# Optimization experiments

Hardware: AMD Instinct MI355X
Metric: run time of the kernel (lower is better)

## Reference

```python
import math
import jax, jax.numpy as jnp
import numpy as np

B, C, H, W = 2, 256, 256, 256
TH, TW = 256, 256
U = V = 2            # window_size
PE_DIM = 256
DIM = 256
HEADS = 8
TEMP = 10000.0


def sine_pe(y, x, num_pos_feats, temp, card):
    """Faithful port of get_sine_position_encoding (use_norm=True)."""
    eps = 1e-6
    scale = 2.0 * math.pi
    y = y / (card[0] + eps) * scale
    x = x / (card[1] + eps) * scale
    dt = jnp.arange(num_pos_feats, dtype=jnp.float32)
    dim_t = temp ** (2.0 * jnp.floor(dt / 2.0) / num_pos_feats)
    px = x[..., None] / dim_t
    py = y[..., None] / dim_t

    def interleave(p):
        s = jnp.stack((jnp.sin(p[..., 0::2]), jnp.cos(p[..., 1::2])), axis=-1)
        return s.reshape(s.shape[:-2] + (-1,))

    return jnp.concatenate((interleave(py), interleave(px)), axis=-1)


def setup_inputs() -> dict:
    key = jax.random.key(0)
    ks = jax.random.split(key, 8)
    return {
        "feat_supp": jax.random.normal(ks[0], (B, C, H, W), jnp.float32),
        "offset": jax.random.normal(ks[1], (B, TH, TW, 2), jnp.float32) * 2.0,
        "Wq": jax.random.normal(ks[2], (DIM, PE_DIM), jnp.float32) * 0.02,
        "bq": jax.random.normal(ks[3], (DIM,), jnp.float32) * 0.02,
        "Wk": jax.random.normal(ks[4], (DIM, PE_DIM), jnp.float32) * 0.02,
        "bk": jax.random.normal(ks[5], (DIM,), jnp.float32) * 0.02,
        "Wv": jax.random.normal(ks[6], (DIM, PE_DIM), jnp.float32) * 0.02,
        "bv": jax.random.normal(ks[7], (DIM,), jnp.float32) * 0.02,
    }


def reference(feat_supp, offset, Wq, bq, Wk, bk, Wv, bv):
    UV = U * V
    THW = TH * TW
    Dh = DIM // HEADS
    attn_scale = Dh ** (-0.5)
    d = PE_DIM // C  # = 1 here

    # --- warp grid: integer window corners + fractional residual ---
    tgt = jnp.stack(jnp.meshgrid(jnp.arange(TH), jnp.arange(TW), indexing='ij'), axis=-1)  # [TH,TW,2]
    win = jnp.stack(jnp.meshgrid(jnp.arange(U), jnp.arange(V), indexing='ij'), axis=-1)    # [U,V,2]
    full = tgt[None].astype(jnp.float32) + offset[..., ::-1]            # [B,TH,TW,2]
    intg = jnp.floor(full).astype(jnp.int32)
    deci = (full - intg.astype(full.dtype)).reshape(B, THW, 2)          # fractional part
    idx = (intg[:, :, :, None, None, :] + win[None, None, None]).reshape(B, THW * UV, 2)

    # --- duplicate-padding gather (gather_hw) ---
    h_idx = jnp.clip(idx[..., 0], 0, H - 1)
    w_idx = jnp.clip(idx[..., 1], 0, W - 1)
    feat = feat_supp.transpose(0, 2, 3, 1).reshape(B, H * W, C)
    lin = h_idx * W + w_idx                                             # [B, THW*UV]
    feat_warp = jnp.take_along_axis(feat, lin[:, :, None], axis=1)      # [B, THW*UV, C]
    feat_warp_ori = feat_warp.reshape(B, THW, UV, C, 1)

    # --- sine PE on window coords (card = window_size - 1) ---
    ye, xe = jnp.meshgrid(jnp.arange(U, dtype=jnp.float32), jnp.arange(V, dtype=jnp.float32), indexing='ij')
    pos_bias = sine_pe(ye.reshape(1, -1), xe.reshape(1, -1), PE_DIM // 2, TEMP, (U - 1, V - 1))  # [1,UV,PE_DIM]
    pe_warp = pos_bias.reshape(1, 1, UV, C, d)
    fw = (feat_warp_ori + pe_warp).reshape(B, THW, UV, PE_DIM)

    # --- query features: window mean + sine PE of fractional offset (card = window_size) ---
    feat_base = feat_warp_ori[..., 0].mean(axis=2)                      # [B,THW,C]
    pe_curr = sine_pe(deci[..., 0], deci[..., 1], PE_DIM // 2, TEMP, (U, V)).reshape(B, THW, C, d)
    fb = (feat_base[..., None] + pe_curr).reshape(B, THW, PE_DIM)

    # --- cross attention: 1 query vs UV keys per target pixel ---
    q = (fb @ Wq.T + bq).reshape(B, THW, HEADS, Dh)
    k = (fw @ Wk.T + bk).reshape(B, THW, UV, HEADS, Dh)
    v = (fw @ Wv.T + bv).reshape(B, THW, UV, HEADS, Dh)
    attn = jnp.einsum('bthd,btuhd->bthu', q * attn_scale, k)
    attn = jax.nn.softmax(attn, axis=-1)
    out = jnp.einsum('bthu,btuhd->bthd', attn, v).reshape(B, TH, TW, DIM)
    return out.transpose(0, 3, 1, 2)                                    # [B, DIM, TH, TW]
```

## Files before the change

kernel.cpp:

```cpp
#include <hip/hip_runtime.h>


using short8 = __attribute__((ext_vector_type(8))) short;
using uint4v = __attribute__((ext_vector_type(4))) unsigned;
using f32x4  = __attribute__((ext_vector_type(4))) float;
typedef unsigned short u16;

#define LOG2_1E4 13.287712379549449f
#define TWO_PI   6.283185307179586f
#define ATT_SCL  0.17677669529663687f

__device__ __forceinline__ float bs2f(u16 s) {
    unsigned u = ((unsigned)s) << 16;
    float f; __builtin_memcpy(&f, &u, 4); return f;
}
__device__ __forceinline__ u16 f2bs(float f) {
    unsigned u; __builtin_memcpy(&u, &f, 4);
    u += 0x7fffu + ((u >> 16) & 1u);
    return (u16)(u >> 16);
}
__device__ __forceinline__ unsigned cvt_pk_bf16(float lo, float hi) {
    unsigned r;
    asm("v_cvt_pk_bf16_f32 %0, %1, %2" : "=v"(r) : "v"(lo), "v"(hi));
    return r;
}

__device__ __forceinline__ int probe_is_f32(const u16* offs_raw) {
    const int lane = threadIdx.x & 63;
    const float v = bs2f(offs_raw[lane * 2]);
    const float av = fabsf(v);
    const bool insane = !(av >= 1e-3f && av <= 1000.0f);
    return __popcll(__ballot(insane)) >= 16 ? 1 : 0;
}

__global__ __launch_bounds__(256) void irm_canon(
    const void* offs_raw, const void* Wq_r, const void* bq_r,
    const void* Wk_r, const void* bk_r, const void* Wv_r, const void* bv_r,
    unsigned char* canon)
{
    const int is_f32 = probe_is_f32((const u16*)offs_raw);
    float* offsC = (float*)canon;
    u16* WqC = (u16*)(canon + (1u << 20));
    u16* WkC = (u16*)(canon + (1u << 20) + (1u << 17));
    u16* WvC = (u16*)(canon + (1u << 20) + (2u << 17));
    u16* bqC = (u16*)(canon + (1u << 20) + (3u << 17));
    u16* bkC = bqC + 256;
    u16* bvC = bkC + 256;

    const int gid = blockIdx.x * 256 + threadIdx.x;
    if (gid < 262144) {
        offsC[gid] = is_f32 ? ((const float*)offs_raw)[gid]
                            : bs2f(((const u16*)offs_raw)[gid]);
    } else if (gid < 262144 + 3 * 65536) {
        const int r = gid - 262144, w = r >> 16, i = r & 65535;
        const void* src = (w == 0) ? Wq_r : (w == 1) ? Wk_r : Wv_r;
        u16*       dst  = (w == 0) ? WqC  : (w == 1) ? WkC  : WvC;
        dst[i] = is_f32 ? f2bs(((const float*)src)[i]) : ((const u16*)src)[i];
    } else if (gid < 262144 + 3 * 65536 + 3 * 256) {
        const int r = gid - 262144 - 3 * 65536, w = r >> 8, i = r & 255;
        const void* src = (w == 0) ? bq_r : (w == 1) ? bk_r : bv_r;
        u16*       dst  = (w == 0) ? bqC  : (w == 1) ? bkC  : bvC;
        dst[i] = is_f32 ? f2bs(((const float*)src)[i]) : ((const u16*)src)[i];
    }
}

__global__ __launch_bounds__(256) void irm_transpose(const void* __restrict__ feat_raw,
                                                     const u16* __restrict__ offs_raw,
                                                     u16* __restrict__ featT) {
    const int is_f32 = probe_is_f32(offs_raw);
    __shared__ u16 tile[64][72];
    const int b   = blockIdx.z;
    const int c0  = blockIdx.y << 6;
    const int hw0 = blockIdx.x << 6;
    const int tid = threadIdx.x;
    const int r    = tid >> 4;
    const int col4 = (tid & 15) << 2;
    #pragma unroll
    for (int it = 0; it < 4; ++it) {
        const int c = (it << 4) + r;
        const size_t idx = ((size_t)((b << 8) + c0 + c) << 16) + hw0 + col4;
        ushort4 o;
        if (is_f32) {
            const float4 v = *(const float4*)((const float*)feat_raw + idx);
            const unsigned lo = cvt_pk_bf16(v.x, v.y);
            const unsigned hi = cvt_pk_bf16(v.z, v.w);
            o.x = (u16)(lo & 0xffffu); o.y = (u16)(lo >> 16);
            o.z = (u16)(hi & 0xffffu); o.w = (u16)(hi >> 16);
        } else {
            o = *(const ushort4*)((const u16*)feat_raw + idx);
        }
        *(ushort4*)&tile[c][col4 ^ (((c >> 3) & 7) << 3)] = o;
    }
    __syncthreads();
    const int s = tid & 7;
    const int m = tid >> 3;
    #pragma unroll
    for (int it2 = 0; it2 < 2; ++it2) {
        const int hw = (it2 << 5) + m;
        short8 o;
        #pragma unroll
        for (int k = 0; k < 8; ++k) {
            const int c = (s << 3) + k;
            o[k] = (short)tile[c][hw ^ (((c >> 3) & 7) << 3)];
        }
        u16* dst = featT + (((size_t)((b << 16) + hw0 + hw)) << 8) + c0 + (s << 3);
        *(short8*)dst = o;
    }
}

__global__ __launch_bounds__(256, 3) void irm_main(
    const void* __restrict__ fsrc,
    const int transposed,
    const u16* __restrict__ offs_raw,
    const float* __restrict__ offsC,
    const u16* __restrict__ Wq, const u16* __restrict__ bq,
    const u16* __restrict__ Wk, const u16* __restrict__ bk_unused,
    const u16* __restrict__ Wv, const u16* __restrict__ bv,
    void* __restrict__ out_raw)
{
    const int is_f32 = probe_is_f32(offs_raw);

    __shared__ __align__(16) unsigned char smem[52992];
    float* pe1    = (float*)smem;
    float* invtab = (float*)(smem + 1024);
    float* sA     = (float*)smem;
    u16*   sFw    = (u16*)(smem + 2304);
    u16*   sV     = (u16*)(smem + 2304);
    u16*   sFb    = (u16*)(smem + 36096);
    u16*   sQ     = (u16*)(smem + 44544);

    const int tid = threadIdx.x;
    const int raw = blockIdx.x;
    const int wq_ = ((raw & 7) << 10) | (raw >> 3);
    const int b   = wq_ >> 12;
    const int t0  = (wq_ & 4095) << 4;

    const int p0 = tid >> 4;
    const int cx = tid & 15;
    const int t  = t0 + p0;
    const float offx = offsC[((((size_t)b << 16) + (size_t)t) << 1) + 0];
    const float offy = offsC[((((size_t)b << 16) + (size_t)t) << 1) + 1];

    {
        const int c = tid;
        const int j = (c & 127) >> 1;
        const float invt = exp2f(-(float)j * (LOG2_1E4 / 64.0f));
        const float arg = (TWO_PI / (1.0f + 1e-6f)) * invt;
        pe1[c]    = (c & 1) ? __cosf(arg) : __sinf(arg);
        invtab[c] = invt;
    }
    __syncthreads();

    {
        const int ty = t >> 8, tx = t & 255;
        const float fy = (float)ty + offy;
        const float fx = (float)tx + offx;
        const float fiy = floorf(fy), fix = floorf(fx);
        const int iy = (int)fiy, ix = (int)fix;
        const float dy = fy - fiy, dx = fx - fix;

        int lin4[4];
        #pragma unroll
        for (int u = 0; u < 4; ++u) {
            int hy = iy + (u >> 1); hy = hy < 0 ? 0 : (hy > 255 ? 255 : hy);
            int wx = ix + (u & 1);  wx = wx < 0 ? 0 : (wx > 255 ? 255 : wx);
            lin4[u] = (hy << 8) | wx;
        }

        short8 g[4][2];
        if (transposed) {
            #pragma unroll
            for (int u = 0; u < 4; ++u) {
                const u16* src = (const u16*)fsrc +
                    ((((size_t)(b << 16)) + (size_t)lin4[u]) << 8) + (cx << 4);
                g[u][0] = *(const short8*)(src);
                g[u][1] = *(const short8*)(src + 8);
            }
        } else {
            #pragma unroll
            for (int u = 0; u < 4; ++u) {
                #pragma unroll
                for (int i = 0; i < 8; ++i) {
                    const size_t i0 = (((size_t)((b << 8) + (cx << 4) + i)) << 16) + lin4[u];
                    const size_t i1 = (((size_t)((b << 8) + (cx << 4) + 8 + i)) << 16) + lin4[u];
                    g[u][0][i] = is_f32 ? (short)f2bs(((const float*)fsrc)[i0]) : (short)((const u16*)fsrc)[i0];
                    g[u][1][i] = is_f32 ? (short)f2bs(((const float*)fsrc)[i1]) : (short)((const u16*)fsrc)[i1];
                }
            }
        }

        float pe1v[16], invtv[16];
        #pragma unroll
        for (int i = 0; i < 16; ++i) {
            pe1v[i]  = pe1[(cx << 4) + i];
            invtv[i] = invtab[(cx << 4) + i];
        }

        const bool hi_half = (cx >= 8);
        float gsum[16];
        #pragma unroll
        for (int i = 0; i < 16; ++i) gsum[i] = 0.0f;

        #pragma unroll
        for (int u = 0; u < 4; ++u) {
            const bool sel = hi_half ? (bool)(u & 1) : (bool)(u >> 1);
            unsigned pk[8];
            #pragma unroll
            for (int i2 = 0; i2 < 8; ++i2) {
                float w2[2];
                #pragma unroll
                for (int k = 0; k < 2; ++k) {
                    const int i = i2 * 2 + k;
                    const float f = bs2f((u16)g[u][i >> 3][i & 7]);
                    gsum[i] += f;
                    const float pz = (i & 1) ? 1.0f : 0.0f;
                    w2[k] = f + (sel ? pe1v[i] : pz);
                }
                pk[i2] = cvt_pk_bf16(w2[0], w2[1]);
            }
            const uint4v lo = {pk[0], pk[1], pk[2], pk[3]};
            const uint4v hi = {pk[4], pk[5], pk[6], pk[7]};
            *(uint4v*)&sFw[((p0 << 2) + u) * 264 + (cx << 4)]     = lo;
            *(uint4v*)&sFw[((p0 << 2) + u) * 264 + (cx << 4) + 8] = hi;
        }

        const float ys = dy * (TWO_PI / (2.0f + 1e-6f));
        const float xs = dx * (TWO_PI / (2.0f + 1e-6f));
        const float sxy = hi_half ? xs : ys;
        unsigned qk[8];
        #pragma unroll
        for (int i2 = 0; i2 < 8; ++i2) {
            float v2[2];
            #pragma unroll
            for (int k = 0; k < 2; ++k) {
                const int i = i2 * 2 + k;
                const float arg = sxy * invtv[i];
                const float pe = (i & 1) ? __cosf(arg) : __sinf(arg);
                v2[k] = gsum[i] * 0.25f + pe;
            }
            qk[i2] = cvt_pk_bf16(v2[0], v2[1]);
        }
        const uint4v qlo = {qk[0], qk[1], qk[2], qk[3]};
        const uint4v qhi = {qk[4], qk[5], qk[6], qk[7]};
        *(uint4v*)&sFb[p0 * 264 + (cx << 4)]     = qlo;
        *(uint4v*)&sFb[p0 * 264 + (cx << 4) + 8] = qhi;
    }
    __syncthreads();

    const int lane = tid & 63;
    const int wv   = tid >> 6;
    const int c15  = lane & 15;
    const int qd   = lane >> 4;
    const int colbase = wv << 6;
    const f32x4 zero4 = {0.f, 0.f, 0.f, 0.f};

    {
        f32x4 accQ[4];
        #pragma unroll
        for (int nt = 0; nt < 4; ++nt) accQ[nt] = zero4;
        #pragma unroll
        for (int ks = 0; ks < 8; ++ks) {
            short8 aq = *(const short8*)&sFb[c15 * 264 + ks * 32 + qd * 8];
            #pragma unroll
            for (int nt = 0; nt < 4; ++nt) {
                short8 bw = *(const short8*)&Wq[(colbase + nt * 16 + c15) * 256 + ks * 32 + qd * 8];
                accQ[nt] = __builtin_amdgcn_mfma_f32_16x16x32_bf16(aq, bw, accQ[nt], 0, 0, 0);
            }
        }
        #pragma unroll
        for (int nt = 0; nt < 4; ++nt) {
            const int n = colbase + nt * 16 + c15;
            const float bias = bs2f(bq[n]);
            #pragma unroll
            for (int rp = 0; rp < 2; ++rp) {
                const unsigned pk = cvt_pk_bf16(accQ[nt][2 * rp] + bias, accQ[nt][2 * rp + 1] + bias);
                sQ[(qd * 4 + 2 * rp)     * 264 + n] = (u16)(pk & 0xffffu);
                sQ[(qd * 4 + 2 * rp + 1) * 264 + n] = (u16)(pk >> 16);
            }
        }
    }
    asm volatile("" ::: "memory");

    f32x4 accK[4][4];
    #pragma unroll
    for (int m = 0; m < 4; ++m)
        #pragma unroll
        for (int nt = 0; nt < 4; ++nt) accK[m][nt] = zero4;
    #pragma unroll
    for (int ks = 0; ks < 8; ++ks) {
        short8 af[4], bfr[4];
        #pragma unroll
        for (int m = 0; m < 4; ++m)
            af[m] = *(const short8*)&sFw[(m * 16 + c15) * 264 + ks * 32 + qd * 8];
        #pragma unroll
        for (int nt = 0; nt < 4; ++nt)
            bfr[nt] = *(const short8*)&Wk[(colbase + nt * 16 + c15) * 256 + ks * 32 + qd * 8];
        #pragma unroll
        for (int m = 0; m < 4; ++m)
            #pragma unroll
            for (int nt = 0; nt < 4; ++nt)
                accK[m][nt] = __builtin_amdgcn_mfma_f32_16x16x32_bf16(af[m], bfr[nt], accK[m][nt], 0, 0, 0);
    }

    {
        float part[4][4][2];
        #pragma unroll
        for (int m = 0; m < 4; ++m)
            #pragma unroll
            for (int r = 0; r < 4; ++r) { part[m][r][0] = 0.f; part[m][r][1] = 0.f; }
        #pragma unroll
        for (int m = 0; m < 4; ++m) {
            #pragma unroll
            for (int nt = 0; nt < 4; ++nt) {
                const float qv = bs2f(sQ[(4 * m + qd) * 264 + colbase + nt * 16 + c15]);
                #pragma unroll
                for (int r = 0; r < 4; ++r)
                    part[m][r][nt >> 1] += accK[m][nt][r] * qv;
            }
        }
        #pragma unroll
        for (int m = 0; m < 4; ++m)
            #pragma unroll
            for (int r = 0; r < 4; ++r)
                #pragma unroll
                for (int h2 = 0; h2 < 2; ++h2) {
                    float v = part[m][r][h2];
                    v += __shfl_xor(v, 1);
                    v += __shfl_xor(v, 2);
                    v += __shfl_xor(v, 4);
                    v += __shfl_xor(v, 8);
                    part[m][r][h2] = v;
                }
        auto smax_write = [&](const float (&pm)[4][2], const int p) {
            #pragma unroll
            for (int h2 = 0; h2 < 2; ++h2) {
                const float l0 = pm[0][h2] * ATT_SCL, l1 = pm[1][h2] * ATT_SCL;
                const float l2 = pm[2][h2] * ATT_SCL, l3 = pm[3][h2] * ATT_SCL;
                const float mx = fmaxf(fmaxf(l0, l1), fmaxf(l2, l3));
                const float e0 = __expf(l0 - mx), e1 = __expf(l1 - mx);
                const float e2 = __expf(l2 - mx), e3 = __expf(l3 - mx);
                const float inv = __fdividef(1.0f, e0 + e1 + e2 + e3);
                float* ap = &sA[p * 36 + ((wv << 1) + h2) * 4];
                ap[0] = e0 * inv; ap[1] = e1 * inv; ap[2] = e2 * inv; ap[3] = e3 * inv;
            }
        };
        if      (c15 == 0) { smax_write(part[0], qd);     smax_write(part[1], 4 + qd);  }
        else if (c15 == 8) { smax_write(part[2], 8 + qd); smax_write(part[3], 12 + qd); }
    }

    f32x4 accV[4][4];
    #pragma unroll
    for (int m = 0; m < 4; ++m)
        #pragma unroll
        for (int nt = 0; nt < 4; ++nt) accV[m][nt] = zero4;
    #pragma unroll
    for (int ks = 0; ks < 8; ++ks) {
        short8 af[4], bfr[4];
        #pragma unroll
        for (int m = 0; m < 4; ++m)
            af[m] = *(const short8*)&sFw[(m * 16 + c15) * 264 + ks * 32 + qd * 8];
        #pragma unroll
        for (int nt = 0; nt < 4; ++nt)
            bfr[nt] = *(const short8*)&Wv[(colbase + nt * 16 + c15) * 256 + ks * 32 + qd * 8];
        #pragma unroll
        for (int m = 0; m < 4; ++m)
            #pragma unroll
            for (int nt = 0; nt < 4; ++nt)
                accV[m][nt] = __builtin_amdgcn_mfma_f32_16x16x32_bf16(af[m], bfr[nt], accV[m][nt], 0, 0, 0);
    }
    __syncthreads();

    #pragma unroll
    for (int nt = 0; nt < 4; ++nt) {
        const int n = colbase + nt * 16 + c15;
        const float bias = bs2f(bv[n]);
        #pragma unroll
        for (int m = 0; m < 4; ++m) {
            #pragma unroll
            for (int rp = 0; rp < 2; ++rp) {
                const int row = m * 16 + qd * 4 + 2 * rp;
                const int ns = n ^ (((row >> 2) & 7) << 3);
                const unsigned pk = cvt_pk_bf16(accV[m][nt][2 * rp] + bias, accV[m][nt][2 * rp + 1] + bias);
                sV[row * 264 + ns]       = (u16)(pk & 0xffffu);
                sV[(row + 1) * 264 + ns] = (u16)(pk >> 16);
            }
        }
    }
    __syncthreads();

    {
        const int p  = tid & 15;
        const int h  = (tid >> 4) & 7;
        const int dh = tid >> 7;
        const f32x4 a4 = *(const f32x4*)&sA[p * 36 + h * 4];
        float acc[16];
        #pragma unroll
        for (int i = 0; i < 16; ++i) acc[i] = 0.0f;
        #pragma unroll
        for (int u = 0; u < 4; ++u) {
            const int row = p * 4 + u;
            const int f = ((row >> 2) & 7) << 3;
            const int cb = h * 32 + dh * 16;
            const short8 v0 = *(const short8*)&sV[row * 264 + (cb ^ f)];
            const short8 v1 = *(const short8*)&sV[row * 264 + ((cb + 8) ^ f)];
            const float a = a4[u];
            #pragma unroll
            for (int i = 0; i < 8; ++i) {
                acc[i]     += a * bs2f((u16)v0[i]);
                acc[i + 8] += a * bs2f((u16)v1[i]);
            }
        }
        const size_t base = (((size_t)((b << 8) + h * 32 + dh * 16)) << 16) + t0 + p;
        if (is_f32) {
            float* dst = (float*)out_raw + base;
            #pragma unroll
            for (int i = 0; i < 16; ++i)
                __builtin_nontemporal_store(acc[i], dst + ((size_t)i << 16));
        } else {
            u16* dst = (u16*)out_raw + base;
            #pragma unroll
            for (int i = 0; i < 16; ++i)
                __builtin_nontemporal_store(f2bs(acc[i]), dst + ((size_t)i << 16));
        }
    }
}

extern "C" void kernel_launch(void* const* d_in, const int* in_sizes, int n_in,
                              void* d_out, int out_size, void* d_ws, size_t ws_size,
                              hipStream_t stream) {
    const size_t FEATT_BYTES = (size_t)1 << 26;
    const size_t CANON_BYTES = (1u << 20) + (3u << 17) + 3 * 512;
    const int use_t = (ws_size >= FEATT_BYTES + CANON_BYTES) ? 1 : 0;

    unsigned char* ws    = (unsigned char*)d_ws;
    unsigned char* canon = ws + (use_t ? FEATT_BYTES : 0);
    float* offsC = (float*)canon;
    u16* WqC = (u16*)(canon + (1u << 20));
    u16* WkC = (u16*)(canon + (1u << 20) + (1u << 17));
    u16* WvC = (u16*)(canon + (1u << 20) + (2u << 17));
    u16* bqC = (u16*)(canon + (1u << 20) + (3u << 17));
    u16* bkC = bqC + 256;
    u16* bvC = bkC + 256;

    irm_canon<<<1795, 256, 0, stream>>>(d_in[1], d_in[2], d_in[3], d_in[4],
                                        d_in[5], d_in[6], d_in[7], canon);
    if (use_t)
        irm_transpose<<<dim3(1024, 4, 2), 256, 0, stream>>>(d_in[0], (const u16*)d_in[1], (u16*)ws);
    irm_main<<<dim3(8192), 256, 0, stream>>>(use_t ? (const void*)ws : d_in[0], use_t,
                                             (const u16*)d_in[1], offsC,
                                             WqC, bqC, WkC, bkC, WvC, bvC, d_out);
}
```

Measured before the change: 610.6 us.

## Transpose MFMA operands to keep Q/K/V in registers and drop LDS round-trips

Swaps the MFMA operand roles so weights are the A operand and features the B operand. Each lane then holds Q, K and V for one pixel column, which lets attention logits, softmax and the weighted V sum run entirely in registers with small cross-lane shuffles. The sQ/sA/sV shared buffers, the extra barriers and the per-block PE table setup (now computed per thread with sincos) go away, and the feature tiles use an XOR-swizzled layout. Shared memory drops enough to raise the occupancy hint to 4 blocks per CU. In exchange, output stores become strided per lane and are no longer nontemporal, and register pressure may limit the higher occupancy.

```diff
diff --git a/kernel.cpp b/kernel.cpp
--- a/kernel.cpp
+++ b/kernel.cpp
@@ -108,7 +108,7 @@
     }
 }
 
-__global__ __launch_bounds__(256, 3) void irm_main(
+__global__ __launch_bounds__(256, 4) void irm_main(
     const void* __restrict__ fsrc,
     const int transposed,
     const u16* __restrict__ offs_raw,
@@ -120,14 +120,9 @@
 {
     const int is_f32 = probe_is_f32(offs_raw);
 
-    __shared__ __align__(16) unsigned char smem[52992];
-    float* pe1    = (float*)smem;
-    float* invtab = (float*)(smem + 1024);
-    float* sA     = (float*)smem;
-    u16*   sFw    = (u16*)(smem + 2304);
-    u16*   sV     = (u16*)(smem + 2304);
-    u16*   sFb    = (u16*)(smem + 36096);
-    u16*   sQ     = (u16*)(smem + 44544);
+    __shared__ __align__(16) unsigned char smem[40960];
+    u16* sFb = (u16*)smem;
+    u16* sFw = (u16*)(smem + 8192);
 
     const int tid = threadIdx.x;
     const int raw = blockIdx.x;
@@ -140,16 +135,6 @@
     const int t  = t0 + p0;
     const float offx = offsC[((((size_t)b << 16) + (size_t)t) << 1) + 0];
     const float offy = offsC[((((size_t)b << 16) + (size_t)t) << 1) + 1];
-
-    {
-        const int c = tid;
-        const int j = (c & 127) >> 1;
-        const float invt = exp2f(-(float)j * (LOG2_1E4 / 64.0f));
-        const float arg = (TWO_PI / (1.0f + 1e-6f)) * invt;
-        pe1[c]    = (c & 1) ? __cosf(arg) : __sinf(arg);
-        invtab[c] = invt;
-    }
-    __syncthreads();
 
     {
         const int ty = t >> 8, tx = t & 255;
@@ -189,11 +174,13 @@
             }
         }
 
-        float pe1v[16], invtv[16];
-        #pragma unroll
-        for (int i = 0; i < 16; ++i) {
-            pe1v[i]  = pe1[(cx << 4) + i];
-            invtv[i] = invtab[(cx << 4) + i];
+        float invt[8], s1[8], c1[8];
+        #pragma unroll
+        for (int a = 0; a < 8; ++a) {
+            const int j = ((cx << 3) + a) & 63;
+            invt[a] = exp2f(-(float)j * (LOG2_1E4 / 64.0f));
+            const float arg = (TWO_PI / (1.0f + 1e-6f)) * invt[a];
+            __sincosf(arg, &s1[a], &c1[a]);
         }
 
         const bool hi_half = (cx >= 8);
@@ -206,22 +193,21 @@
             const bool sel = hi_half ? (bool)(u & 1) : (bool)(u >> 1);
             unsigned pk[8];
             #pragma unroll
-            for (int i2 = 0; i2 < 8; ++i2) {
-                float w2[2];
-                #pragma unroll
-                for (int k = 0; k < 2; ++k) {
-                    const int i = i2 * 2 + k;
-                    const float f = bs2f((u16)g[u][i >> 3][i & 7]);
-                    gsum[i] += f;
-                    const float pz = (i & 1) ? 1.0f : 0.0f;
-                    w2[k] = f + (sel ? pe1v[i] : pz);
-                }
-                pk[i2] = cvt_pk_bf16(w2[0], w2[1]);
-            }
+            for (int a = 0; a < 8; ++a) {
+                const float f0 = bs2f((u16)g[u][a >> 2][(2 * a) & 7]);
+                const float f1 = bs2f((u16)g[u][a >> 2][(2 * a + 1) & 7]);
+                gsum[2 * a]     += f0;
+                gsum[2 * a + 1] += f1;
+                const float w0 = f0 + (sel ? s1[a] : 0.0f);
+                const float w1 = f1 + (sel ? c1[a] : 1.0f);
+                pk[a] = cvt_pk_bf16(w0, w1);
+            }
+            const int row = (p0 << 2) + u;
+            const int rp  = row ^ ((row >> 3) & 7);
             const uint4v lo = {pk[0], pk[1], pk[2], pk[3]};
             const uint4v hi = {pk[4], pk[5], pk[6], pk[7]};
-            *(uint4v*)&sFw[((p0 << 2) + u) * 264 + (cx << 4)]     = lo;
-            *(uint4v*)&sFw[((p0 << 2) + u) * 264 + (cx << 4) + 8] = hi;
+            *(uint4v*)&sFw[(((2 * cx) * 64 + rp)) * 8]     = lo;
+            *(uint4v*)&sFw[(((2 * cx + 1) * 64 + rp)) * 8] = hi;
         }
 
         const float ys = dy * (TWO_PI / (2.0f + 1e-6f));
@@ -229,21 +215,16 @@
         const float sxy = hi_half ? xs : ys;
         unsigned qk[8];
         #pragma unroll
-        for (int i2 = 0; i2 < 8; ++i2) {
-            float v2[2];
-            #pragma unroll
-            for (int k = 0; k < 2; ++k) {
-                const int i = i2 * 2 + k;
-                const float arg = sxy * invtv[i];
-                const float pe = (i & 1) ? __cosf(arg) : __sinf(arg);
-                v2[k] = gsum[i] * 0.25f + pe;
-            }
-            qk[i2] = cvt_pk_bf16(v2[0], v2[1]);
-        }
+        for (int a = 0; a < 8; ++a) {
+            float s2, c2;
+            __sincosf(sxy * invt[a], &s2, &c2);
+            qk[a] = cvt_pk_bf16(gsum[2 * a] * 0.25f + s2, gsum[2 * a + 1] * 0.25f + c2);
+        }
+        const int rb = p0 ^ (cx & 7);
         const uint4v qlo = {qk[0], qk[1], qk[2], qk[3]};
         const uint4v qhi = {qk[4], qk[5], qk[6], qk[7]};
-        *(uint4v*)&sFb[p0 * 264 + (cx << 4)]     = qlo;
-        *(uint4v*)&sFb[p0 * 264 + (cx << 4) + 8] = qhi;
+        *(uint4v*)&sFb[((2 * cx) * 16 + rb) * 8]     = qlo;
+        *(uint4v*)&sFb[((2 * cx + 1) * 16 + rb) * 8] = qhi;
     }
     __syncthreads();
 
@@ -253,174 +234,119 @@
     const int qd   = lane >> 4;
     const int colbase = wv << 6;
     const f32x4 zero4 = {0.f, 0.f, 0.f, 0.f};
-
+    const int kwkey = (c15 >> 1) & 7;
+    const int krow0 = 4 * c15;
+
+    f32x4 accQt[4];
+    #pragma unroll
+    for (int nt = 0; nt < 4; ++nt) accQt[nt] = zero4;
+    #pragma unroll
+    for (int ks = 0; ks < 8; ++ks) {
+        const int gidx = ks * 4 + qd;
+        const short8 bfb = *(const short8*)&sFb[(gidx * 16 + (c15 ^ ((gidx >> 1) & 7))) * 8];
+        #pragma unroll
+        for (int nt = 0; nt < 4; ++nt) {
+            const short8 aw = *(const short8*)&Wq[(colbase + nt * 16 + c15) * 256 + ks * 32 + qd * 8];
+            accQt[nt] = __builtin_amdgcn_mfma_f32_16x16x32_bf16(aw, bfb, accQt[nt], 0, 0, 0);
+        }
+    }
+    #pragma unroll
+    for (int nt = 0; nt < 4; ++nt) {
+        const ushort4 b4 = *(const ushort4*)&bq[colbase + nt * 16 + qd * 4];
+        accQt[nt][0] += bs2f(b4.x); accQt[nt][1] += bs2f(b4.y);
+        accQt[nt][2] += bs2f(b4.z); accQt[nt][3] += bs2f(b4.w);
+    }
+
+    f32x4 accKt[4][4];
+    #pragma unroll
+    for (int u = 0; u < 4; ++u)
+        #pragma unroll
+        for (int nt = 0; nt < 4; ++nt) accKt[u][nt] = zero4;
+    #pragma unroll
+    for (int ks = 0; ks < 8; ++ks) {
+        short8 aw[4];
+        #pragma unroll
+        for (int nt = 0; nt < 4; ++nt)
+            aw[nt] = *(const short8*)&Wk[(colbase + nt * 16 + c15) * 256 + ks * 32 + qd * 8];
+        #pragma unroll
+        for (int u = 0; u < 4; ++u) {
+            const short8 bf = *(const short8*)&sFw[((ks * 4 + qd) * 64 + ((krow0 + u) ^ kwkey)) * 8];
+            #pragma unroll
+            for (int nt = 0; nt < 4; ++nt)
+                accKt[u][nt] = __builtin_amdgcn_mfma_f32_16x16x32_bf16(aw[nt], bf, accKt[u][nt], 0, 0, 0);
+        }
+    }
+
+    float att[4][2];
     {
-        f32x4 accQ[4];
-        #pragma unroll
-        for (int nt = 0; nt < 4; ++nt) accQ[nt] = zero4;
-        #pragma unroll
-        for (int ks = 0; ks < 8; ++ks) {
-            short8 aq = *(const short8*)&sFb[c15 * 264 + ks * 32 + qd * 8];
-            #pragma unroll
-            for (int nt = 0; nt < 4; ++nt) {
-                short8 bw = *(const short8*)&Wq[(colbase + nt * 16 + c15) * 256 + ks * 32 + qd * 8];
-                accQ[nt] = __builtin_amdgcn_mfma_f32_16x16x32_bf16(aq, bw, accQ[nt], 0, 0, 0);
-            }
-        }
-        #pragma unroll
-        for (int nt = 0; nt < 4; ++nt) {
-            const int n = colbase + nt * 16 + c15;
-            const float bias = bs2f(bq[n]);
-            #pragma unroll
-            for (int rp = 0; rp < 2; ++rp) {
-                const unsigned pk = cvt_pk_bf16(accQ[nt][2 * rp] + bias, accQ[nt][2 * rp + 1] + bias);
-                sQ[(qd * 4 + 2 * rp)     * 264 + n] = (u16)(pk & 0xffffu);
-                sQ[(qd * 4 + 2 * rp + 1) * 264 + n] = (u16)(pk >> 16);
-            }
-        }
-    }
-    asm volatile("" ::: "memory");
-
-    f32x4 accK[4][4];
-    #pragma unroll
-    for (int m = 0; m < 4; ++m)
-        #pragma unroll
-        for (int nt = 0; nt < 4; ++nt) accK[m][nt] = zero4;
+        float lg[4][2];
+        #pragma unroll
+        for (int u = 0; u < 4; ++u) {
+            #pragma unroll
+            for (int h2 = 0; h2 < 2; ++h2) {
+                float acc = 0.0f;
+                #pragma unroll
+                for (int ntl = 0; ntl < 2; ++ntl) {
+                    const int nt = h2 * 2 + ntl;
+                    #pragma unroll
+                    for (int r = 0; r < 4; ++r)
+                        acc += accQt[nt][r] * accKt[u][nt][r];
+                }
+                acc += __shfl_xor(acc, 16);
+                acc += __shfl_xor(acc, 32);
+                lg[u][h2] = acc * ATT_SCL;
+            }
+        }
+        #pragma unroll
+        for (int h2 = 0; h2 < 2; ++h2) {
+            const float mx = fmaxf(fmaxf(lg[0][h2], lg[1][h2]), fmaxf(lg[2][h2], lg[3][h2]));
+            float e[4], es = 0.0f;
+            #pragma unroll
+            for (int u = 0; u < 4; ++u) { e[u] = __expf(lg[u][h2] - mx); es += e[u]; }
+            const float inv = __fdividef(1.0f, es);
+            #pragma unroll
+            for (int u = 0; u < 4; ++u) att[u][h2] = e[u] * inv;
+        }
+    }
+
+    f32x4 accVt[4][4];
+    #pragma unroll
+    for (int u = 0; u < 4; ++u)
+        #pragma unroll
+        for (int nt = 0; nt < 4; ++nt) accVt[u][nt] = zero4;
     #pragma unroll
     for (int ks = 0; ks < 8; ++ks) {
-        short8 af[4], bfr[4];
-        #pragma unroll
-        for (int m = 0; m < 4; ++m)
-            af[m] = *(const short8*)&sFw[(m * 16 + c15) * 264 + ks * 32 + qd * 8];
+        short8 aw[4];
         #pragma unroll
         for (int nt = 0; nt < 4; ++nt)
-            bfr[nt] = *(const short8*)&Wk[(colbase + nt * 16 + c15) * 256 + ks * 32 + qd * 8];
-        #pragma unroll
-        for (int m = 0; m < 4; ++m)
+            aw[nt] = *(const short8*)&Wv[(colbase + nt * 16 + c15) * 256 + ks * 32 + qd * 8];
+        #pragma unroll
+        for (int u = 0; u < 4; ++u) {
+            const short8 bf = *(const short8*)&sFw[((ks * 4 + qd) * 64 + ((krow0 + u) ^ kwkey)) * 8];
             #pragma unroll
             for (int nt = 0; nt < 4; ++nt)
-                accK[m][nt] = __builtin_amdgcn_mfma_f32_16x16x32_bf16(af[m], bfr[nt], accK[m][nt], 0, 0, 0);
-    }
-
-    {
-        float part[4][4][2];
-        #pragma unroll
-        for (int m = 0; m < 4; ++m)
-            #pragma unroll
-            for (int r = 0; r < 4; ++r) { part[m][r][0] = 0.f; part[m][r][1] = 0.f; }
-        #pragma unroll
-        for (int m = 0; m < 4; ++m) {
-            #pragma unroll
-            for (int nt = 0; nt < 4; ++nt) {
-                const float qv = bs2f(sQ[(4 * m + qd) * 264 + colbase + nt * 16 + c15]);
-                #pragma unroll
-                for (int r = 0; r < 4; ++r)
-                    part[m][r][nt >> 1] += accK[m][nt][r] * qv;
-            }
-        }
-        #pragma unroll
-        for (int m = 0; m < 4; ++m)
-            #pragma unroll
-            for (int r = 0; r < 4; ++r)
-                #pragma unroll
-                for (int h2 = 0; h2 < 2; ++h2) {
-                    float v = part[m][r][h2];
-                    v += __shfl_xor(v, 1);
-                    v += __shfl_xor(v, 2);
-                    v += __shfl_xor(v, 4);
-                    v += __shfl_xor(v, 8);
-                    part[m][r][h2] = v;
-                }
-        auto smax_write = [&](const float (&pm)[4][2], const int p) {
-            #pragma unroll
-            for (int h2 = 0; h2 < 2; ++h2) {
-                const float l0 = pm[0][h2] * ATT_SCL, l1 = pm[1][h2] * ATT_SCL;
-                const float l2 = pm[2][h2] * ATT_SCL, l3 = pm[3][h2] * ATT_SCL;
-                const float mx = fmaxf(fmaxf(l0, l1), fmaxf(l2, l3));
-                const float e0 = __expf(l0 - mx), e1 = __expf(l1 - mx);
-                const float e2 = __expf(l2 - mx), e3 = __expf(l3 - mx);
-                const float inv = __fdividef(1.0f, e0 + e1 + e2 + e3);
-                float* ap = &sA[p * 36 + ((wv << 1) + h2) * 4];
-                ap[0] = e0 * inv; ap[1] = e1 * inv; ap[2] = e2 * inv; ap[3] = e3 * inv;
-            }
-        };
-        if      (c15 == 0) { smax_write(part[0], qd);     smax_write(part[1], 4 + qd);  }
-        else if (c15 == 8) { smax_write(part[2], 8 + qd); smax_write(part[3], 12 + qd); }
-    }
-
-    f32x4 accV[4][4];
-    #pragma unroll
-    for (int m = 0; m < 4; ++m)
-        #pragma unroll
-        for (int nt = 0; nt < 4; ++nt) accV[m][nt] = zero4;
-    #pragma unroll
-    for (int ks = 0; ks < 8; ++ks) {
-        short8 af[4], bfr[4];
-        #pragma unroll
-        for (int m = 0; m < 4; ++m)
-            af[m] = *(const short8*)&sFw[(m * 16 + c15) * 264 + ks * 32 + qd * 8];
-        #pragma unroll
-        for (int nt = 0; nt < 4; ++nt)
-            bfr[nt] = *(const short8*)&Wv[(colbase + nt * 16 + c15) * 256 + ks * 32 + qd * 8];
-        #pragma unroll
-        for (int m = 0; m < 4; ++m)
-            #pragma unroll
-            for (int nt = 0; nt < 4; ++nt)
-                accV[m][nt] = __builtin_amdgcn_mfma_f32_16x16x32_bf16(af[m], bfr[nt], accV[m][nt], 0, 0, 0);
-    }
-    __syncthreads();
+                accVt[u][nt] = __builtin_amdgcn_mfma_f32_16x16x32_bf16(aw[nt], bf, accVt[u][nt], 0, 0, 0);
+        }
+    }
 
     #pragma unroll
     for (int nt = 0; nt < 4; ++nt) {
-        const int n = colbase + nt * 16 + c15;
-        const float bias = bs2f(bv[n]);
-        #pragma unroll
-        for (int m = 0; m < 4; ++m) {
-            #pragma unroll
-            for (int rp = 0; rp < 2; ++rp) {
-                const int row = m * 16 + qd * 4 + 2 * rp;
-                const int ns = n ^ (((row >> 2) & 7) << 3);
-                const unsigned pk = cvt_pk_bf16(accV[m][nt][2 * rp] + bias, accV[m][nt][2 * rp + 1] + bias);
-                sV[row * 264 + ns]       = (u16)(pk & 0xffffu);
-                sV[(row + 1) * 264 + ns] = (u16)(pk >> 16);
-            }
-        }
-    }
-    __syncthreads();
-
-    {
-        const int p  = tid & 15;
-        const int h  = (tid >> 4) & 7;
-        const int dh = tid >> 7;
-        const f32x4 a4 = *(const f32x4*)&sA[p * 36 + h * 4];
-        float acc[16];
-        #pragma unroll
-        for (int i = 0; i < 16; ++i) acc[i] = 0.0f;
-        #pragma unroll
-        for (int u = 0; u < 4; ++u) {
-            const int row = p * 4 + u;
-            const int f = ((row >> 2) & 7) << 3;
-            const int cb = h * 32 + dh * 16;
-            const short8 v0 = *(const short8*)&sV[row * 264 + (cb ^ f)];
-            const short8 v1 = *(const short8*)&sV[row * 264 + ((cb + 8) ^ f)];
-            const float a = a4[u];
-            #pragma unroll
-            for (int i = 0; i < 8; ++i) {
-                acc[i]     += a * bs2f((u16)v0[i]);
-                acc[i + 8] += a * bs2f((u16)v1[i]);
-            }
-        }
-        const size_t base = (((size_t)((b << 8) + h * 32 + dh * 16)) << 16) + t0 + p;
-        if (is_f32) {
-            float* dst = (float*)out_raw + base;
-            #pragma unroll
-            for (int i = 0; i < 16; ++i)
-                __builtin_nontemporal_store(acc[i], dst + ((size_t)i << 16));
-        } else {
-            u16* dst = (u16*)out_raw + base;
-            #pragma unroll
-            for (int i = 0; i < 16; ++i)
-                __builtin_nontemporal_store(f2bs(acc[i]), dst + ((size_t)i << 16));
+        const int h2 = nt >> 1;
+        const ushort4 bv4 = *(const ushort4*)&bv[colbase + nt * 16 + qd * 4];
+        const float bvf[4] = {bs2f(bv4.x), bs2f(bv4.y), bs2f(bv4.z), bs2f(bv4.w)};
+        const int cbase = (b << 8) + colbase + nt * 16 + qd * 4;
+        #pragma unroll
+        for (int r = 0; r < 4; ++r) {
+            float val = att[0][h2] * accVt[0][nt][r];
+            val += att[1][h2] * accVt[1][nt][r];
+            val += att[2][h2] * accVt[2][nt][r];
+            val += att[3][h2] * accVt[3][nt][r];
+            val += bvf[r];
+            if (is_f32) {
+                ((float*)out_raw)[(((size_t)(cbase + r)) << 16) + t0 + c15] = val;
+            } else {
+                ((u16*)out_raw)[(((size_t)(cbase + r)) << 16) + t0 + c15] = f2bs(val);
+            }
         }
     }
 }
```

Result: slower. 1.457 ms (+138.6%).
